# Performance work log

Hardware: AMD Instinct MI355X
Metric: run time of the kernel (lower is better)

## Reference

```python
import jax, jax.numpy as jnp
import numpy as np


def setup_inputs() -> dict:
    key = jax.random.key(0)
    k1, k2 = jax.random.split(key)
    N, D, G = 1048576, 128, 1024
    features = jax.random.normal(k1, (N, D), dtype=jnp.float32)
    # sorted node->graph assignment, equivalent to torch.split by batch_num_nodes
    segment_ids = jnp.sort(jax.random.randint(k2, (N,), 0, G, dtype=jnp.int32))
    return {"features": features, "segment_ids": segment_ids, "num_graphs": G}


def reference(features, segment_ids, num_graphs):
    # Single fused segment-sum pass: sums node features per graph and stacks
    # into [num_graphs, d_feat], same math as split + per-chunk torch.sum + stack.
    return jax.ops.segment_sum(
        features, segment_ids, num_segments=num_graphs, indices_are_sorted=True
    )
```

## Files before the change

kernel.cpp:

```cpp
#include <hip/hip_runtime.h>
#include <hip/hip_bf16.h>


typedef float v4f __attribute__((ext_vector_type(4)));

__global__ __launch_bounds__(256) void seg_boundaries_kernel(
    const int* __restrict__ seg, int* __restrict__ offs, int N, int G) {
    int i = blockIdx.x * blockDim.x + threadIdx.x;
    if (i >= N) return;
    int s = seg[i];
    int prev = (i == 0) ? -1 : seg[i - 1];
    for (int g = prev + 1; g <= s; ++g) offs[g] = i;
    if (i == N - 1) {
        for (int g = s + 1; g <= G; ++g) offs[g] = N;
    }
}

__global__ __launch_bounds__(256) void SumPooling_54700703482382_kernel(
    const v4f* __restrict__ feat,
    const int* __restrict__ offs,
    v4f*       __restrict__ out) {
    const int g     = blockIdx.x;
    const int start = offs[g];
    const int end   = offs[g + 1];

    const int tid   = threadIdx.x;
    const int c     = tid & 31;
    const int rlane = tid >> 5;

    v4f acc = (v4f)(0.f);
    const v4f* p = feat + (size_t)start * 32 + (size_t)rlane * 32 + c;
    int iters = (end - start - rlane + 7) >> 3;

    #pragma unroll 8
    for (int it = 0; it < iters; ++it) {
        v4f v = __builtin_nontemporal_load(p);
        acc += v;
        p += 8 * 32;
    }

    __shared__ v4f red[256];
    red[tid] = acc;
    __syncthreads();
    if (tid < 128) red[tid] += red[tid + 128];
    __syncthreads();
    if (tid < 64) red[tid] += red[tid + 64];
    __syncthreads();
    if (tid < 32) {
        v4f r0 = red[tid] + red[tid + 32];
        out[(size_t)g * 32 + tid] = r0;
    }
}

extern "C" void kernel_launch(void* const* d_in, const int* in_sizes, int n_in,
                              void* d_out, int out_size, void* d_ws, size_t ws_size,
                              hipStream_t stream) {
    const v4f* feat = (const v4f*)d_in[0];
    const int* seg  = (const int*)d_in[1];
    v4f*       out  = (v4f*)d_out;

    const int N = in_sizes[1];
    const int D = in_sizes[0] / N;
    const int G = out_size / D;

    int* offs = (int*)d_ws;

    seg_boundaries_kernel<<<(N + 255) / 256, 256, 0, stream>>>(seg, offs, N, G);
    SumPooling_54700703482382_kernel<<<G, 256, 0, stream>>>(feat, offs, out);
}
```

Measured before the change: 91.33 us.

## Replace boundary kernel with in-block wave-parallel binary search over segment ids

Removes the separate segment-boundary kernel, which read all N segment ids and wrote an offsets array. Each pooling block now finds its own start and end rows with a 64-way ballot-based search over the sorted ids, run by two waves. This drops one kernel launch and a full pass over the ids, at the cost of a few dependent global-load rounds before each block can start its feature loads. The output store also becomes nontemporal.

```diff
diff --git a/kernel.cpp b/kernel.cpp
--- a/kernel.cpp
+++ b/kernel.cpp
@@ -4,27 +4,44 @@
 
 typedef float v4f __attribute__((ext_vector_type(4)));
 
-__global__ __launch_bounds__(256) void seg_boundaries_kernel(
-    const int* __restrict__ seg, int* __restrict__ offs, int N, int G) {
-    int i = blockIdx.x * blockDim.x + threadIdx.x;
-    if (i >= N) return;
-    int s = seg[i];
-    int prev = (i == 0) ? -1 : seg[i - 1];
-    for (int g = prev + 1; g <= s; ++g) offs[g] = i;
-    if (i == N - 1) {
-        for (int g = s + 1; g <= G; ++g) offs[g] = N;
+__device__ __forceinline__ int wave_lower_bound(const int* __restrict__ seg,
+                                                int N, int x) {
+    const int lane = threadIdx.x & 63;
+    int lo = 0, hi = N;
+    while (hi > lo) {
+        int w    = hi - lo;
+        int step = (w + 63) >> 6;
+        int q    = lo + lane * step;
+        bool pred = (q < hi) && (seg[q] < x);
+        unsigned long long m = __ballot(pred);
+        int c = __popcll(m);
+        if (c == 0) { hi = lo; break; }
+        int nhi = lo + c * step;
+        if (nhi > hi) nhi = hi;
+        lo = lo + (c - 1) * step + 1;
+        hi = nhi;
     }
+    return lo;
 }
 
 __global__ __launch_bounds__(256) void SumPooling_54700703482382_kernel(
     const v4f* __restrict__ feat,
-    const int* __restrict__ offs,
-    v4f*       __restrict__ out) {
-    const int g     = blockIdx.x;
-    const int start = offs[g];
-    const int end   = offs[g + 1];
+    const int* __restrict__ seg,
+    v4f*       __restrict__ out,
+    int N) {
+    const int g    = blockIdx.x;
+    const int tid  = threadIdx.x;
+    const int wave = tid >> 6;
 
-    const int tid   = threadIdx.x;
+    __shared__ int sb[2];
+    if (wave < 2) {
+        int r = wave_lower_bound(seg, N, g + wave);
+        if ((tid & 63) == 0) sb[wave] = r;
+    }
+    __syncthreads();
+    const int start = sb[0];
+    const int end   = sb[1];
+
     const int c     = tid & 31;
     const int rlane = tid >> 5;
 
@@ -48,7 +65,7 @@
     __syncthreads();
     if (tid < 32) {
         v4f r0 = red[tid] + red[tid + 32];
-        out[(size_t)g * 32 + tid] = r0;
+        __builtin_nontemporal_store(r0, &out[(size_t)g * 32 + tid]);
     }
 }
 
@@ -63,8 +80,5 @@
     const int D = in_sizes[0] / N;
     const int G = out_size / D;
 
-    int* offs = (int*)d_ws;
-
-    seg_boundaries_kernel<<<(N + 255) / 256, 256, 0, stream>>>(seg, offs, N, G);
-    SumPooling_54700703482382_kernel<<<G, 256, 0, stream>>>(feat, offs, out);
+    SumPooling_54700703482382_kernel<<<G, 256, 0, stream>>>(feat, seg, out, N);
 }
```

Result: faster. 88.44 us (-3.2%).
